# Kernel optimization log

Hardware: AMD Instinct MI355X
Metric: run time of the kernel (lower is better)

Reference implementation:

```python
import jax, jax.numpy as jnp
import numpy as np

B, N, D, H, DK, DV, R = 4, 256, 256, 8, 32, 32, 64
EPS = 1e-6


def setup_inputs() -> dict:
    key = jax.random.key(0)
    ks = jax.random.split(key, 16)
    s = D ** -0.5
    return {
        "q": jax.random.normal(ks[0], (B, N, D), jnp.float32),
        "k": jax.random.normal(ks[1], (B, N, D), jnp.float32),
        "v": jax.random.normal(ks[2], (B, N, D), jnp.float32),
        "mask": jax.random.randint(ks[3], (B, N, N), 0, 2).astype(jnp.int32),
        "link": jax.random.uniform(ks[4], (B, N, N, R), jnp.float32),
        "Wq": jax.random.normal(ks[5], (D, H * DK), jnp.float32) * s,
        "Wk": jax.random.normal(ks[6], (D, H * DK), jnp.float32) * s,
        "Wr": jax.random.normal(ks[7], (D, H * DK), jnp.float32) * s,
        "Wv": jax.random.normal(ks[8], (D, H * DV), jnp.float32) * s,
        "Wvv": jax.random.normal(ks[9], (D, H * DV), jnp.float32) * s,
        "relationE": jax.random.normal(ks[10], (R, D), jnp.float32) * s,
        "Wo": jax.random.normal(ks[11], (H * DV, D), jnp.float32) * s,
        "gamma": jnp.ones((D,), jnp.float32),
        "beta": jnp.zeros((D,), jnp.float32),
    }


def reference(q, k, v, mask, link, Wq, Wk, Wr, Wv, Wvv, relationE, Wo, gamma, beta):
    # rela_num != 0 branch of Ruleformer MultiHeadAttention (dropout = identity, eval mode).
    residual = q
    b, n, d = q.shape
    # per-head projections of X (== q == residual in this branch): [b,h,n,dk]
    Xq = (q @ Wq).reshape(b, n, H, DK).transpose(0, 2, 1, 3)
    Xk = (q @ Wk).reshape(b, n, H, DK).transpose(0, 2, 1, 3)
    Xv = (q @ Wv).reshape(b, n, H, DV).transpose(0, 2, 1, 3)

    # calcE: relation-biased scores. Rk[b,i,j,h,d] = (link @ relationE @ Wr)
    Rk = jnp.einsum('bijr,re->bije', link, relationE @ Wr).reshape(b, n, n, H, DK)
    # attn[b,h,i,j] = Xq[b,h,i] . (Xk[b,h,j] + Rk[b,i,j,h])
    attn = jnp.einsum('bhid,bhjd->bhij', Xq, Xk)
    attn = attn + jnp.einsum('bijhd,bhid->bhij', Rk, Xq)
    attn = attn / (DK ** 0.5)
    attn = jnp.where(mask[:, None, :, :] == 0, -1e9, attn)
    alpha = jax.nn.softmax(attn, axis=-1)  # [b,h,n,n]

    # calcZ: Z[b,h,i] = sum_j alpha[b,h,i,j] * (Xv[b,h,j] + Rv[b,i,j,h])
    Rv = jnp.einsum('bijr,re->bije', link, relationE @ Wvv).reshape(b, n, n, H, DV)
    Z = jnp.einsum('bhij,bhjd->bhid', alpha, Xv)
    Z = Z + jnp.einsum('bhij,bijhd->bhid', alpha, Rv)

    out = Z.transpose(0, 2, 1, 3).reshape(b, n, H * DV) @ Wo
    out = out + residual
    mu = out.mean(-1, keepdims=True)
    var = ((out - mu) ** 2).mean(-1, keepdims=True)
    out = (out - mu) * jax.lax.rsqrt(var + EPS) * gamma + beta
    return out, alpha
```

## Files before the change

kernel.cpp:

```cpp
#include <hip/hip_runtime.h>
#include <math.h>

constexpr int B_ = 4, N_ = 256, D_ = 256, H_ = 8, DK_ = 32, DV_ = 32, R_ = 64;
constexpr float SCALE_ = 0.17677669529663687f;
constexpr float EPS_ = 1e-6f;

__global__ __launch_bounds__(256) void ekev_kernel(
        const float* __restrict__ relE, const float* __restrict__ Wr,
        const float* __restrict__ Wvv, float* __restrict__ Ek,
        float* __restrict__ Ev) {
    int r = blockIdx.x & 63;
    int which = blockIdx.x >> 6;
    const float* W = which ? Wvv : Wr;
    float* out = which ? Ev : Ek;
    __shared__ float row[256];
    int tid = threadIdx.x;
    row[tid] = relE[r * 256 + tid];
    __syncthreads();
    float acc = 0.f;
    for (int d = 0; d < 256; ++d) acc += row[d] * W[d * 256 + tid];
    out[r * 256 + tid] = acc;
}

__global__ __launch_bounds__(256) void mcat_kernel(
        const float* __restrict__ Wq, const float* __restrict__ Ek,
        float* __restrict__ M) {
    int d = blockIdx.x;
    int t = threadIdx.x;
    __shared__ float wrow[256];
    wrow[t] = Wq[d * 256 + t];
    __syncthreads();
    for (int hr = t; hr < 512; hr += 256) {
        int h = hr >> 6, r = hr & 63;
        const float4* ek4 = (const float4*)(Ek + r * 256 + h * 32);
        const float4* w4 = (const float4*)(wrow + h * 32);
        float acc = 0.f;
#pragma unroll
        for (int k = 0; k < 8; ++k) {
            float4 e = ek4[k], w = w4[k];
            acc += e.x * w.x + e.y * w.y + e.z * w.z + e.w * w.w;
        }
        M[d * 512 + hr] = acc;
    }
}

__global__ __launch_bounds__(256) void projT_kernel(
        const float* __restrict__ q, const float* __restrict__ Wq,
        const float* __restrict__ Wk, const float* __restrict__ Wv,
        const float* __restrict__ M, float* __restrict__ Xq,
        float* __restrict__ Xk, float* __restrict__ Xv,
        float* __restrict__ T) {
    int ct = blockIdx.x >> 4, rt = blockIdx.x & 15;
    int t = threadIdx.x;
    __shared__ float ash[32 * 65];
    __shared__ float bsh[32 * 64];
    const float* W;
    int ncols, cbase;
    if (ct < 4)       { W = Wq; cbase = ct * 64;        ncols = 256; }
    else if (ct < 8)  { W = Wk; cbase = (ct - 4) * 64;  ncols = 256; }
    else if (ct < 12) { W = Wv; cbase = (ct - 8) * 64;  ncols = 256; }
    else              { W = M;  cbase = (ct - 12) * 64; ncols = 512; }
    int ti = t >> 4, tj = t & 15;
    float acc[4][4] = {{0.f}};
    for (int kc = 0; kc < 8; ++kc) {
        __syncthreads();
#pragma unroll
        for (int kk = 0; kk < 2; ++kk) {
            int m = t + kk * 256;
            int i = m >> 3, kq = m & 7;
            float4 v = *(const float4*)(q + (size_t)(rt * 64 + i) * 256 + kc * 32 + kq * 4);
            ash[(kq * 4 + 0) * 65 + i] = v.x;
            ash[(kq * 4 + 1) * 65 + i] = v.y;
            ash[(kq * 4 + 2) * 65 + i] = v.z;
            ash[(kq * 4 + 3) * 65 + i] = v.w;
        }
#pragma unroll
        for (int kk = 0; kk < 2; ++kk) {
            int m = t + kk * 256;
            int k = m >> 4, j4 = m & 15;
            float4 v = *(const float4*)(W + (size_t)(kc * 32 + k) * ncols + cbase + j4 * 4);
            *(float4*)(bsh + k * 64 + j4 * 4) = v;
        }
        __syncthreads();
#pragma unroll 8
        for (int k = 0; k < 32; ++k) {
            float4 av = *(const float4*)(ash + k * 65 + ti * 4);
            float4 bv = *(const float4*)(bsh + k * 64 + tj * 4);
            acc[0][0] += av.x * bv.x; acc[0][1] += av.x * bv.y;
            acc[0][2] += av.x * bv.z; acc[0][3] += av.x * bv.w;
            acc[1][0] += av.y * bv.x; acc[1][1] += av.y * bv.y;
            acc[1][2] += av.y * bv.z; acc[1][3] += av.y * bv.w;
            acc[2][0] += av.z * bv.x; acc[2][1] += av.z * bv.y;
            acc[2][2] += av.z * bv.z; acc[2][3] += av.z * bv.w;
            acc[3][0] += av.w * bv.x; acc[3][1] += av.w * bv.y;
            acc[3][2] += av.w * bv.z; acc[3][3] += av.w * bv.w;
        }
    }
    if (ct < 12) {
        float* dst = (ct < 4) ? Xq : (ct < 8) ? Xk : Xv;
        int gcol = (ct & 3) * 64 + tj * 4;
        int h = gcol >> 5, dk = gcol & 31;
#pragma unroll
        for (int a = 0; a < 4; ++a) {
            int row = rt * 64 + ti * 4 + a;
            int bb = row >> 8, n = row & 255;
            *(float4*)(dst + ((size_t)(bb * 8 + h) * 256 + n) * 32 + dk) =
                make_float4(acc[a][0], acc[a][1], acc[a][2], acc[a][3]);
        }
    } else {
        int gcol = (ct - 12) * 64 + tj * 4;
#pragma unroll
        for (int a = 0; a < 4; ++a) {
            int row = rt * 64 + ti * 4 + a;
            *(float4*)(T + (size_t)row * 512 + gcol) =
                make_float4(acc[a][0], acc[a][1], acc[a][2], acc[a][3]);
        }
    }
}

__global__ __launch_bounds__(256) void qk_kernel(
        const float* __restrict__ Xq, const float* __restrict__ Xk,
        float* __restrict__ qk) {
    int x = blockIdx.x;
    int jt = x & 3, it = (x >> 2) & 3, bh = x >> 4;
    int t = threadIdx.x;
    __shared__ float xqsh[32 * 64];
    __shared__ float xksh[32 * 64];
#pragma unroll
    for (int k = 0; k < 2; ++k) {
        int m = t + k * 256;
        int i = m >> 3, dq4 = m & 7;
        float4 v = *(const float4*)(Xq + ((size_t)(bh * 256 + it * 64 + i)) * 32 + dq4 * 4);
        xqsh[(dq4 * 4 + 0) * 64 + i] = v.x;
        xqsh[(dq4 * 4 + 1) * 64 + i] = v.y;
        xqsh[(dq4 * 4 + 2) * 64 + i] = v.z;
        xqsh[(dq4 * 4 + 3) * 64 + i] = v.w;
        float4 u = *(const float4*)(Xk + ((size_t)(bh * 256 + jt * 64 + i)) * 32 + dq4 * 4);
        xksh[(dq4 * 4 + 0) * 64 + i] = u.x;
        xksh[(dq4 * 4 + 1) * 64 + i] = u.y;
        xksh[(dq4 * 4 + 2) * 64 + i] = u.z;
        xksh[(dq4 * 4 + 3) * 64 + i] = u.w;
    }
    __syncthreads();
    int ti = t >> 4, tj = t & 15;
    float acc[4][4] = {{0.f}};
#pragma unroll 8
    for (int dk = 0; dk < 32; ++dk) {
        float4 av = *(const float4*)(xqsh + dk * 64 + ti * 4);
        float4 bv = *(const float4*)(xksh + dk * 64 + tj * 4);
        acc[0][0] += av.x * bv.x; acc[0][1] += av.x * bv.y;
        acc[0][2] += av.x * bv.z; acc[0][3] += av.x * bv.w;
        acc[1][0] += av.y * bv.x; acc[1][1] += av.y * bv.y;
        acc[1][2] += av.y * bv.z; acc[1][3] += av.y * bv.w;
        acc[2][0] += av.z * bv.x; acc[2][1] += av.z * bv.y;
        acc[2][2] += av.z * bv.z; acc[2][3] += av.z * bv.w;
        acc[3][0] += av.w * bv.x; acc[3][1] += av.w * bv.y;
        acc[3][2] += av.w * bv.z; acc[3][3] += av.w * bv.w;
    }
#pragma unroll
    for (int a = 0; a < 4; ++a) {
        int i = it * 64 + ti * 4 + a;
        *(float4*)(qk + ((size_t)(bh * 256 + i)) * 256 + jt * 64 + tj * 4) =
            make_float4(acc[a][0], acc[a][1], acc[a][2], acc[a][3]);
    }
}

__global__ __launch_bounds__(256) void biassm_kernel(
        const float* __restrict__ link, const float* __restrict__ Tg,
        const float* __restrict__ qk, const int* __restrict__ mask,
        float* __restrict__ alpha, float* __restrict__ S) {
    int bi = blockIdx.x;
    int b = bi >> 8, i = bi & 255;
    int t = threadIdx.x;
    __shared__ float Tsh[512];
    __shared__ float ashm[2048];
    __shared__ float part[2048];
    __shared__ float redsh[64];
    Tsh[t] = Tg[(size_t)bi * 512 + t];
    Tsh[256 + t] = Tg[(size_t)bi * 512 + 256 + t];

    float qv[8];
#pragma unroll
    for (int h = 0; h < 8; ++h)
        qv[h] = qk[((size_t)(b * 8 + h) * 256 + i) * 256 + t];
    int mv = mask[((size_t)(b * 256 + i)) * 256 + t];
    __syncthreads();

    float s[8] = {0.f, 0.f, 0.f, 0.f, 0.f, 0.f, 0.f, 0.f};
    {
        const float4* l4 = (const float4*)(link + ((size_t)(bi * 256 + t)) * 64);
        const float4* T4 = (const float4*)Tsh;
#pragma unroll 4
        for (int k = 0; k < 16; ++k) {
            float4 lv = l4[k];
#pragma unroll
            for (int h = 0; h < 8; ++h) {
                float4 tv = T4[h * 16 + k];
                s[h] += lv.x * tv.x + lv.y * tv.y + lv.z * tv.z + lv.w * tv.w;
            }
        }
    }
#pragma unroll
    for (int h = 0; h < 8; ++h) {
        s[h] = (qv[h] + s[h]) * SCALE_;
        if (mv == 0) s[h] = -1e9f;
    }

    int lane = t & 63, wv = t >> 6;
#pragma unroll
    for (int h = 0; h < 8; ++h) {
        float v = s[h];
        for (int off = 32; off > 0; off >>= 1) v = fmaxf(v, __shfl_xor(v, off));
        if (lane == 0) redsh[h * 4 + wv] = v;
    }
    __syncthreads();
    float mx[8];
#pragma unroll
    for (int h = 0; h < 8; ++h)
        mx[h] = fmaxf(fmaxf(redsh[h * 4 + 0], redsh[h * 4 + 1]),
                      fmaxf(redsh[h * 4 + 2], redsh[h * 4 + 3]));
#pragma unroll
    for (int h = 0; h < 8; ++h) {
        float e = __expf(s[h] - mx[h]);
        s[h] = e;
        float v = e;
        for (int off = 32; off > 0; off >>= 1) v += __shfl_xor(v, off);
        if (lane == 0) redsh[32 + h * 4 + wv] = v;
    }
    __syncthreads();
#pragma unroll
    for (int h = 0; h < 8; ++h) {
        float esum = redsh[32 + h * 4 + 0] + redsh[32 + h * 4 + 1] +
                     redsh[32 + h * 4 + 2] + redsh[32 + h * 4 + 3];
        float a = s[h] * (1.f / esum);
        ashm[h * 256 + t] = a;
        alpha[((size_t)(b * 8 + h) * 256 + i) * 256 + t] = a;
    }
    __syncthreads();

    int r = t & 63, g = t >> 6;
    float pacc2[8] = {0.f, 0.f, 0.f, 0.f, 0.f, 0.f, 0.f, 0.f};
    const float* lp2 = link + ((size_t)(bi * 256 + g * 64)) * 64 + r;
#pragma unroll 4
    for (int j4 = 0; j4 < 16; ++j4) {
        float l0 = lp2[(j4 * 4 + 0) * 64];
        float l1 = lp2[(j4 * 4 + 1) * 64];
        float l2 = lp2[(j4 * 4 + 2) * 64];
        float l3 = lp2[(j4 * 4 + 3) * 64];
#pragma unroll
        for (int h = 0; h < 8; ++h) {
            float4 a = *(const float4*)(ashm + h * 256 + g * 64 + j4 * 4);
            pacc2[h] += a.x * l0 + a.y * l1 + a.z * l2 + a.w * l3;
        }
    }
#pragma unroll
    for (int h = 0; h < 8; ++h) part[g * 512 + h * 64 + r] = pacc2[h];
    __syncthreads();
    for (int hr = t; hr < 512; hr += 256) {
        S[(size_t)bi * 512 + hr] =
            part[hr] + part[512 + hr] + part[1024 + hr] + part[1536 + hr];
    }
}

__global__ __launch_bounds__(256) void zout_kernel(
        const float* __restrict__ alpha, const float* __restrict__ Xv,
        const float* __restrict__ S, const float* __restrict__ Ev,
        const float* __restrict__ Wo, const float* __restrict__ q,
        const float* __restrict__ gamma, const float* __restrict__ beta,
        float* __restrict__ out) {
    int blk = blockIdx.x;
    int row0 = blk * 2;
    int b = row0 >> 8;
    int t = threadIdx.x;
    __shared__ float Ssh[2 * 512];
    __shared__ float ashm[2 * 2048];
    __shared__ float zsh[2 * 256];
    __shared__ float redsh[16];
    for (int m = t; m < 1024; m += 256)
        Ssh[m] = S[(size_t)(row0 + (m >> 9)) * 512 + (m & 511)];
    for (int m = t; m < 4096; m += 256) {
        int rr = m >> 11, h = (m >> 8) & 7, j = m & 255;
        ashm[m] = alpha[((size_t)(b * 8 + h) * 256 + ((row0 + rr) & 255)) * 256 + j];
    }
    __syncthreads();
    {
        int h = t >> 5, dv = t & 31;
        float z0 = 0.f, z1 = 0.f;
        const float* xv = Xv + ((size_t)(b * 8 + h) * 256) * 32 + dv;
#pragma unroll 4
        for (int j = 0; j < 256; ++j) {
            float x = xv[j * 32];
            z0 += ashm[h * 256 + j] * x;
            z1 += ashm[2048 + h * 256 + j] * x;
        }
#pragma unroll 4
        for (int r = 0; r < 64; ++r) {
            float ev = Ev[r * 256 + h * 32 + dv];
            z0 += Ssh[h * 64 + r] * ev;
            z1 += Ssh[512 + h * 64 + r] * ev;
        }
        zsh[t] = z0;
        zsh[256 + t] = z1;
    }
    __syncthreads();
    float a0 = q[(size_t)row0 * 256 + t];
    float a1 = q[(size_t)(row0 + 1) * 256 + t];
    for (int d4 = 0; d4 < 64; ++d4) {
        float w0 = Wo[(d4 * 4 + 0) * 256 + t];
        float w1 = Wo[(d4 * 4 + 1) * 256 + t];
        float w2 = Wo[(d4 * 4 + 2) * 256 + t];
        float w3 = Wo[(d4 * 4 + 3) * 256 + t];
        float4 z0v = *(const float4*)(zsh + d4 * 4);
        float4 z1v = *(const float4*)(zsh + 256 + d4 * 4);
        a0 += z0v.x * w0 + z0v.y * w1 + z0v.z * w2 + z0v.w * w3;
        a1 += z1v.x * w0 + z1v.y * w1 + z1v.z * w2 + z1v.w * w3;
    }
    int lane = t & 63, wv = t >> 6;
    float acc2[2] = {a0, a1};
#pragma unroll
    for (int rr = 0; rr < 2; ++rr) {
        float v = acc2[rr], v2 = acc2[rr] * acc2[rr];
        for (int off = 32; off > 0; off >>= 1) {
            v += __shfl_xor(v, off);
            v2 += __shfl_xor(v2, off);
        }
        if (lane == 0) {
            redsh[rr * 8 + wv] = v;
            redsh[rr * 8 + 4 + wv] = v2;
        }
    }
    __syncthreads();
#pragma unroll
    for (int rr = 0; rr < 2; ++rr) {
        float sum = redsh[rr * 8 + 0] + redsh[rr * 8 + 1] + redsh[rr * 8 + 2] + redsh[rr * 8 + 3];
        float sum2 = redsh[rr * 8 + 4] + redsh[rr * 8 + 5] + redsh[rr * 8 + 6] + redsh[rr * 8 + 7];
        float mu = sum * (1.f / 256.f);
        float var = sum2 * (1.f / 256.f) - mu * mu;
        float dev = acc2[rr] - mu;
        out[(size_t)(row0 + rr) * 256 + t] = dev * rsqrtf(var + EPS_) * gamma[t] + beta[t];
    }
}

extern "C" void kernel_launch(void* const* d_in, const int* in_sizes, int n_in,
                              void* d_out, int out_size, void* d_ws, size_t ws_size,
                              hipStream_t stream) {
    const float* q     = (const float*)d_in[0];
    const int*   mask  = (const int*)d_in[3];
    const float* link  = (const float*)d_in[4];
    const float* Wq    = (const float*)d_in[5];
    const float* Wk    = (const float*)d_in[6];
    const float* Wr    = (const float*)d_in[7];
    const float* Wv    = (const float*)d_in[8];
    const float* Wvv   = (const float*)d_in[9];
    const float* relE  = (const float*)d_in[10];
    const float* Wo    = (const float*)d_in[11];
    const float* gamma = (const float*)d_in[12];
    const float* beta  = (const float*)d_in[13];

    float* out   = (float*)d_out;
    float* alpha = out + B_ * N_ * D_;

    float* ws    = (float*)d_ws;
    float* Ek    = ws;
    float* Ev    = Ek + 16384;
    float* Mcat  = Ev + 16384;
    float* Xq    = Mcat + 131072;
    float* Xk    = Xq + 262144;
    float* Xv    = Xk + 262144;
    float* T     = Xv + 262144;
    float* qkbuf = T + 524288;
    float* S     = qkbuf + 2097152;

    ekev_kernel<<<128, 256, 0, stream>>>(relE, Wr, Wvv, Ek, Ev);
    mcat_kernel<<<256, 256, 0, stream>>>(Wq, Ek, Mcat);
    projT_kernel<<<320, 256, 0, stream>>>(q, Wq, Wk, Wv, Mcat, Xq, Xk, Xv, T);
    qk_kernel<<<512, 256, 0, stream>>>(Xq, Xk, qkbuf);
    biassm_kernel<<<1024, 256, 0, stream>>>(link, T, qkbuf, mask, alpha, S);
    zout_kernel<<<512, 256, 0, stream>>>(alpha, Xv, S, Ev, Wo, q, gamma, beta, out);
}
```

Baseline: 216.6 us.

## Compute relation bias from Xq·Ek and fuse Z computation into softmax kernel

```diff
diff --git a/kernel.cpp b/kernel.cpp
--- a/kernel.cpp
+++ b/kernel.cpp
@@ -18,48 +18,25 @@
     row[tid] = relE[r * 256 + tid];
     __syncthreads();
     float acc = 0.f;
+#pragma unroll 4
     for (int d = 0; d < 256; ++d) acc += row[d] * W[d * 256 + tid];
     out[r * 256 + tid] = acc;
-}
-
-__global__ __launch_bounds__(256) void mcat_kernel(
-        const float* __restrict__ Wq, const float* __restrict__ Ek,
-        float* __restrict__ M) {
-    int d = blockIdx.x;
-    int t = threadIdx.x;
-    __shared__ float wrow[256];
-    wrow[t] = Wq[d * 256 + t];
-    __syncthreads();
-    for (int hr = t; hr < 512; hr += 256) {
-        int h = hr >> 6, r = hr & 63;
-        const float4* ek4 = (const float4*)(Ek + r * 256 + h * 32);
-        const float4* w4 = (const float4*)(wrow + h * 32);
-        float acc = 0.f;
-#pragma unroll
-        for (int k = 0; k < 8; ++k) {
-            float4 e = ek4[k], w = w4[k];
-            acc += e.x * w.x + e.y * w.y + e.z * w.z + e.w * w.w;
-        }
-        M[d * 512 + hr] = acc;
-    }
 }
 
 __global__ __launch_bounds__(256) void projT_kernel(
         const float* __restrict__ q, const float* __restrict__ Wq,
         const float* __restrict__ Wk, const float* __restrict__ Wv,
-        const float* __restrict__ M, float* __restrict__ Xq,
-        float* __restrict__ Xk, float* __restrict__ Xv,
-        float* __restrict__ T) {
+        float* __restrict__ Xq, float* __restrict__ Xk,
+        float* __restrict__ Xv) {
     int ct = blockIdx.x >> 4, rt = blockIdx.x & 15;
     int t = threadIdx.x;
     __shared__ float ash[32 * 65];
     __shared__ float bsh[32 * 64];
     const float* W;
-    int ncols, cbase;
-    if (ct < 4)       { W = Wq; cbase = ct * 64;        ncols = 256; }
-    else if (ct < 8)  { W = Wk; cbase = (ct - 4) * 64;  ncols = 256; }
-    else if (ct < 12) { W = Wv; cbase = (ct - 8) * 64;  ncols = 256; }
-    else              { W = M;  cbase = (ct - 12) * 64; ncols = 512; }
+    int cbase;
+    if (ct < 4)       { W = Wq; cbase = ct * 64; }
+    else if (ct < 8)  { W = Wk; cbase = (ct - 4) * 64; }
+    else              { W = Wv; cbase = (ct - 8) * 64; }
     int ti = t >> 4, tj = t & 15;
     float acc[4][4] = {{0.f}};
     for (int kc = 0; kc < 8; ++kc) {
@@ -78,7 +55,7 @@
         for (int kk = 0; kk < 2; ++kk) {
             int m = t + kk * 256;
             int k = m >> 4, j4 = m & 15;
-            float4 v = *(const float4*)(W + (size_t)(kc * 32 + k) * ncols + cbase + j4 * 4);
+            float4 v = *(const float4*)(W + (size_t)(kc * 32 + k) * 256 + cbase + j4 * 4);
             *(float4*)(bsh + k * 64 + j4 * 4) = v;
         }
         __syncthreads();
@@ -96,36 +73,29 @@
             acc[3][2] += av.w * bv.z; acc[3][3] += av.w * bv.w;
         }
     }
-    if (ct < 12) {
-        float* dst = (ct < 4) ? Xq : (ct < 8) ? Xk : Xv;
-        int gcol = (ct & 3) * 64 + tj * 4;
-        int h = gcol >> 5, dk = gcol & 31;
-#pragma unroll
-        for (int a = 0; a < 4; ++a) {
-            int row = rt * 64 + ti * 4 + a;
-            int bb = row >> 8, n = row & 255;
-            *(float4*)(dst + ((size_t)(bb * 8 + h) * 256 + n) * 32 + dk) =
-                make_float4(acc[a][0], acc[a][1], acc[a][2], acc[a][3]);
-        }
-    } else {
-        int gcol = (ct - 12) * 64 + tj * 4;
-#pragma unroll
-        for (int a = 0; a < 4; ++a) {
-            int row = rt * 64 + ti * 4 + a;
-            *(float4*)(T + (size_t)row * 512 + gcol) =
-                make_float4(acc[a][0], acc[a][1], acc[a][2], acc[a][3]);
-        }
-    }
-}
-
-__global__ __launch_bounds__(256) void qk_kernel(
+    float* dst = (ct < 4) ? Xq : (ct < 8) ? Xk : Xv;
+    int gcol = (ct & 3) * 64 + tj * 4;
+    int h = gcol >> 5, dk = gcol & 31;
+#pragma unroll
+    for (int a = 0; a < 4; ++a) {
+        int row = rt * 64 + ti * 4 + a;
+        int bb = row >> 8, n = row & 255;
+        *(float4*)(dst + ((size_t)(bb * 8 + h) * 256 + n) * 32 + dk) =
+            make_float4(acc[a][0], acc[a][1], acc[a][2], acc[a][3]);
+    }
+}
+
+__global__ __launch_bounds__(256) void qkT_kernel(
         const float* __restrict__ Xq, const float* __restrict__ Xk,
-        float* __restrict__ qk) {
+        const float* __restrict__ Ek, float* __restrict__ qk,
+        float* __restrict__ T) {
     int x = blockIdx.x;
     int jt = x & 3, it = (x >> 2) & 3, bh = x >> 4;
+    int b = bh >> 3, h = bh & 7;
     int t = threadIdx.x;
     __shared__ float xqsh[32 * 64];
     __shared__ float xksh[32 * 64];
+    __shared__ float eksh[32 * 64];
 #pragma unroll
     for (int k = 0; k < 2; ++k) {
         int m = t + k * 256;
@@ -140,6 +110,18 @@
         xksh[(dq4 * 4 + 1) * 64 + i] = u.y;
         xksh[(dq4 * 4 + 2) * 64 + i] = u.z;
         xksh[(dq4 * 4 + 3) * 64 + i] = u.w;
+    }
+    if (jt == 0) {
+        int r = t >> 2, dq = t & 3;
+#pragma unroll
+        for (int kk = 0; kk < 2; ++kk) {
+            int dq4 = dq + kk * 4;
+            float4 v = *(const float4*)(Ek + r * 256 + h * 32 + dq4 * 4);
+            eksh[(dq4 * 4 + 0) * 64 + r] = v.x;
+            eksh[(dq4 * 4 + 1) * 64 + r] = v.y;
+            eksh[(dq4 * 4 + 2) * 64 + r] = v.z;
+            eksh[(dq4 * 4 + 3) * 64 + r] = v.w;
+        }
     }
     __syncthreads();
     int ti = t >> 4, tj = t & 15;
@@ -163,12 +145,35 @@
         *(float4*)(qk + ((size_t)(bh * 256 + i)) * 256 + jt * 64 + tj * 4) =
             make_float4(acc[a][0], acc[a][1], acc[a][2], acc[a][3]);
     }
-}
-
-__global__ __launch_bounds__(256) void biassm_kernel(
+    if (jt == 0) {
+        float tacc[4][4] = {{0.f}};
+#pragma unroll 8
+        for (int dk = 0; dk < 32; ++dk) {
+            float4 av = *(const float4*)(xqsh + dk * 64 + ti * 4);
+            float4 ev = *(const float4*)(eksh + dk * 64 + tj * 4);
+            tacc[0][0] += av.x * ev.x; tacc[0][1] += av.x * ev.y;
+            tacc[0][2] += av.x * ev.z; tacc[0][3] += av.x * ev.w;
+            tacc[1][0] += av.y * ev.x; tacc[1][1] += av.y * ev.y;
+            tacc[1][2] += av.y * ev.z; tacc[1][3] += av.y * ev.w;
+            tacc[2][0] += av.z * ev.x; tacc[2][1] += av.z * ev.y;
+            tacc[2][2] += av.z * ev.z; tacc[2][3] += av.z * ev.w;
+            tacc[3][0] += av.w * ev.x; tacc[3][1] += av.w * ev.y;
+            tacc[3][2] += av.w * ev.z; tacc[3][3] += av.w * ev.w;
+        }
+#pragma unroll
+        for (int a = 0; a < 4; ++a) {
+            int i = it * 64 + ti * 4 + a;
+            *(float4*)(T + ((size_t)(b * 256 + i)) * 512 + h * 64 + tj * 4) =
+                make_float4(tacc[a][0], tacc[a][1], tacc[a][2], tacc[a][3]);
+        }
+    }
+}
+
+__global__ __launch_bounds__(256) void biassmz_kernel(
         const float* __restrict__ link, const float* __restrict__ Tg,
         const float* __restrict__ qk, const int* __restrict__ mask,
-        float* __restrict__ alpha, float* __restrict__ S) {
+        const float* __restrict__ Xv, const float* __restrict__ Ev,
+        float* __restrict__ alpha, float* __restrict__ Z) {
     int bi = blockIdx.x;
     int b = bi >> 8, i = bi & 255;
     int t = threadIdx.x;
@@ -190,7 +195,7 @@
     {
         const float4* l4 = (const float4*)(link + ((size_t)(bi * 256 + t)) * 64);
         const float4* T4 = (const float4*)Tsh;
-#pragma unroll 4
+#pragma unroll 8
         for (int k = 0; k < 16; ++k) {
             float4 lv = l4[k];
 #pragma unroll
@@ -239,69 +244,54 @@
     __syncthreads();
 
     int r = t & 63, g = t >> 6;
-    float pacc2[8] = {0.f, 0.f, 0.f, 0.f, 0.f, 0.f, 0.f, 0.f};
-    const float* lp2 = link + ((size_t)(bi * 256 + g * 64)) * 64 + r;
+    {
+        float pacc2[8] = {0.f, 0.f, 0.f, 0.f, 0.f, 0.f, 0.f, 0.f};
+        const float* lp2 = link + ((size_t)(bi * 256 + g * 64)) * 64 + r;
 #pragma unroll 4
-    for (int j4 = 0; j4 < 16; ++j4) {
-        float l0 = lp2[(j4 * 4 + 0) * 64];
-        float l1 = lp2[(j4 * 4 + 1) * 64];
-        float l2 = lp2[(j4 * 4 + 2) * 64];
-        float l3 = lp2[(j4 * 4 + 3) * 64];
-#pragma unroll
-        for (int h = 0; h < 8; ++h) {
-            float4 a = *(const float4*)(ashm + h * 256 + g * 64 + j4 * 4);
-            pacc2[h] += a.x * l0 + a.y * l1 + a.z * l2 + a.w * l3;
-        }
-    }
-#pragma unroll
-    for (int h = 0; h < 8; ++h) part[g * 512 + h * 64 + r] = pacc2[h];
-    __syncthreads();
-    for (int hr = t; hr < 512; hr += 256) {
-        S[(size_t)bi * 512 + hr] =
-            part[hr] + part[512 + hr] + part[1024 + hr] + part[1536 + hr];
-    }
-}
-
-__global__ __launch_bounds__(256) void zout_kernel(
-        const float* __restrict__ alpha, const float* __restrict__ Xv,
-        const float* __restrict__ S, const float* __restrict__ Ev,
-        const float* __restrict__ Wo, const float* __restrict__ q,
-        const float* __restrict__ gamma, const float* __restrict__ beta,
-        float* __restrict__ out) {
-    int blk = blockIdx.x;
-    int row0 = blk * 2;
-    int b = row0 >> 8;
-    int t = threadIdx.x;
-    __shared__ float Ssh[2 * 512];
-    __shared__ float ashm[2 * 2048];
-    __shared__ float zsh[2 * 256];
-    __shared__ float redsh[16];
-    for (int m = t; m < 1024; m += 256)
-        Ssh[m] = S[(size_t)(row0 + (m >> 9)) * 512 + (m & 511)];
-    for (int m = t; m < 4096; m += 256) {
-        int rr = m >> 11, h = (m >> 8) & 7, j = m & 255;
-        ashm[m] = alpha[((size_t)(b * 8 + h) * 256 + ((row0 + rr) & 255)) * 256 + j];
-    }
-    __syncthreads();
+        for (int j4 = 0; j4 < 16; ++j4) {
+            float l0 = lp2[(j4 * 4 + 0) * 64];
+            float l1 = lp2[(j4 * 4 + 1) * 64];
+            float l2 = lp2[(j4 * 4 + 2) * 64];
+            float l3 = lp2[(j4 * 4 + 3) * 64];
+#pragma unroll
+            for (int h = 0; h < 8; ++h) {
+                float4 a = *(const float4*)(ashm + h * 256 + g * 64 + j4 * 4);
+                pacc2[h] += a.x * l0 + a.y * l1 + a.z * l2 + a.w * l3;
+            }
+        }
+#pragma unroll
+        for (int h = 0; h < 8; ++h) part[g * 512 + h * 64 + r] = pacc2[h];
+    }
+    __syncthreads();
+    for (int hr = t; hr < 512; hr += 256)
+        Tsh[hr] = part[hr] + part[512 + hr] + part[1024 + hr] + part[1536 + hr];
+    __syncthreads();
+
     {
         int h = t >> 5, dv = t & 31;
-        float z0 = 0.f, z1 = 0.f;
-        const float* xv = Xv + ((size_t)(b * 8 + h) * 256) * 32 + dv;
+        float z = 0.f;
+        const float* ap = ashm + h * 256;
+        const float* xvp = Xv + ((size_t)(b * 8 + h) * 256) * 32 + dv;
 #pragma unroll 4
-        for (int j = 0; j < 256; ++j) {
-            float x = xv[j * 32];
-            z0 += ashm[h * 256 + j] * x;
-            z1 += ashm[2048 + h * 256 + j] * x;
-        }
+        for (int j = 0; j < 256; ++j) z += ap[j] * xvp[j * 32];
+        const float* sp = Tsh + h * 64;
+        const float* evp = Ev + h * 32 + dv;
 #pragma unroll 4
-        for (int r = 0; r < 64; ++r) {
-            float ev = Ev[r * 256 + h * 32 + dv];
-            z0 += Ssh[h * 64 + r] * ev;
-            z1 += Ssh[512 + h * 64 + r] * ev;
-        }
-        zsh[t] = z0;
-        zsh[256 + t] = z1;
-    }
+        for (int rr = 0; rr < 64; ++rr) z += sp[rr] * evp[rr * 256];
+        Z[(size_t)bi * 256 + t] = z;
+    }
+}
+
+__global__ __launch_bounds__(256) void out_kernel(
+        const float* __restrict__ Z, const float* __restrict__ Wo,
+        const float* __restrict__ q, const float* __restrict__ gamma,
+        const float* __restrict__ beta, float* __restrict__ out) {
+    int row0 = blockIdx.x * 2;
+    int t = threadIdx.x;
+    __shared__ float zsh[512];
+    __shared__ float redsh[16];
+    zsh[t] = Z[(size_t)row0 * 256 + t];
+    zsh[256 + t] = Z[(size_t)row0 * 256 + 256 + t];
     __syncthreads();
     float a0 = q[(size_t)row0 * 256 + t];
     float a1 = q[(size_t)(row0 + 1) * 256 + t];
@@ -363,18 +353,16 @@
     float* ws    = (float*)d_ws;
     float* Ek    = ws;
     float* Ev    = Ek + 16384;
-    float* Mcat  = Ev + 16384;
-    float* Xq    = Mcat + 131072;
+    float* Xq    = Ev + 16384;
     float* Xk    = Xq + 262144;
     float* Xv    = Xk + 262144;
     float* T     = Xv + 262144;
     float* qkbuf = T + 524288;
-    float* S     = qkbuf + 2097152;
+    float* Zbuf  = qkbuf + 2097152;
 
     ekev_kernel<<<128, 256, 0, stream>>>(relE, Wr, Wvv, Ek, Ev);
-    mcat_kernel<<<256, 256, 0, stream>>>(Wq, Ek, Mcat);
-    projT_kernel<<<320, 256, 0, stream>>>(q, Wq, Wk, Wv, Mcat, Xq, Xk, Xv, T);
-    qk_kernel<<<512, 256, 0, stream>>>(Xq, Xk, qkbuf);
-    biassm_kernel<<<1024, 256, 0, stream>>>(link, T, qkbuf, mask, alpha, S);
-    zout_kernel<<<512, 256, 0, stream>>>(alpha, Xv, S, Ev, Wo, q, gamma, beta, out);
-}
+    projT_kernel<<<192, 256, 0, stream>>>(q, Wq, Wk, Wv, Xq, Xk, Xv);
+    qkT_kernel<<<512, 256, 0, stream>>>(Xq, Xk, Ek, qkbuf, T);
+    biassmz_kernel<<<1024, 256, 0, stream>>>(link, T, qkbuf, mask, Xv, Ev, alpha, Zbuf);
+    out_kernel<<<512, 256, 0, stream>>>(Zbuf, Wo, q, gamma, beta, out);
+}
```

Result: faster. 208.2 us (-3.9%).
